# Kernel optimization log

Measured on AMD Instinct MI355X. Metric: run time of the kernel, lower is better.

Reference implementation:

```python
import jax, jax.numpy as jnp
import numpy as np

HIDDEN = 256  # C
STE = 128     # D

def setup_inputs() -> dict:
    key = jax.random.key(0)
    ks = jax.random.split(key, 11)
    B, P, Q, N = 8, 96, 96, 1024
    s = 0.02
    return {
        "enc": jax.random.normal(ks[0], (B, P, N, HIDDEN), jnp.float32),
        "ste_enc": jax.random.normal(ks[1], (B, P, N, STE), jnp.float32),
        "ste_dec": jax.random.normal(ks[2], (B, Q, N, STE), jnp.float32),
        "Wq": jax.random.normal(ks[3], (STE, HIDDEN), jnp.float32) * s,
        "bq": jnp.zeros((HIDDEN,), jnp.float32),
        "Wk": jax.random.normal(ks[4], (STE, HIDDEN), jnp.float32) * s,
        "bk": jnp.zeros((HIDDEN,), jnp.float32),
        "Wv": jax.random.normal(ks[5], (HIDDEN, HIDDEN), jnp.float32) * s,
        "bv": jnp.zeros((HIDDEN,), jnp.float32),
        "Wo": jax.random.normal(ks[6], (HIDDEN, HIDDEN), jnp.float32) * s,
        "bo": jnp.zeros((HIDDEN,), jnp.float32),
    }

def reference(enc, ste_enc, ste_dec, Wq, bq, Wk, bk, Wv, bv, Wo, bo):
    # enc: (B,P,N,C), ste_enc: (B,P,N,D), ste_dec: (B,Q,N,D)
    C = enc.shape[-1]
    q = ste_dec @ Wq + bq          # (B,Q,N,H)
    k = ste_enc @ Wk + bk          # (B,P,N,H)
    v = enc @ Wv + bv              # (B,P,N,H)
    # attention per (batch, node): scores (B,N,Q,P)
    scores = jnp.einsum("bqnh,bpnh->bnqp", q, k) / jnp.sqrt(jnp.float32(C))
    attn = jax.nn.softmax(scores, axis=-1)
    out = jnp.einsum("bnqp,bpnh->bqnh", attn, v)  # (B,Q,N,H)
    out = out @ Wo + bo
    return out  # (B,Q,N,C)
```

## Files before the change

### kernel.cpp

```cpp
#include <hip/hip_runtime.h>
#include <stdint.h>

typedef unsigned short u16;
typedef unsigned int u32;
typedef __attribute__((ext_vector_type(8))) short short8;
typedef __attribute__((ext_vector_type(4))) float f32x4;

#define NTHR 384
#define K2E16 0.09016844005556021f

#define KW_OFF    32768
#define KW_STRIDE 272
#define BIAS_OFF  58880
#define BVO_OFF   59264
#define LDS_TOTAL 60288

static __device__ __forceinline__ u16 f2bf(float f) {
  union { float f; u32 u; } v; v.f = f;
  u32 r = v.u + 0x7FFFu + ((v.u >> 16) & 1u);
  return (u16)(r >> 16);
}

__global__ __launch_bounds__(256) void k_setup(
    const float* __restrict__ Wq, const float* __restrict__ Wk,
    const float* __restrict__ Wv, const float* __restrict__ Wo,
    const float* __restrict__ bq,
    const float* __restrict__ bv, const float* __restrict__ bo,
    u16* __restrict__ WkqF, u16* __restrict__ WvoF, float* __restrict__ bvo) {
  const int ci = blockIdx.x;
  const int co = threadIdx.x;
  float acc = 0.f;
  for (int h = 0; h < 256; ++h) acc += Wv[ci*256 + h] * Wo[h*256 + co];
  const int lanepart = ((ci >> 3) & 3)*16 + (co & 15), e = ci & 7;
  const int idxv = (((ci >> 5)*16 + (co >> 4))*64 + lanepart)*8 + e;
  WvoF[idxv] = f2bf(acc);
  if (ci < 128 && co < 144) {
    float a = 0.f;
    if (co < 128)       { for (int h = 0; h < 256; ++h) a += Wk[ci*256 + h] * Wq[co*256 + h]; }
    else if (co == 128) { for (int h = 0; h < 256; ++h) a += Wk[ci*256 + h] * bq[h]; }
    const int idx = (((ci >> 5)*9 + (co >> 4))*64 + lanepart)*8 + e;
    WkqF[idx] = f2bf(a);
  }
  if (ci == 0) {
    float a2 = 0.f;
    for (int h = 0; h < 256; ++h) a2 += bv[h] * Wo[h*256 + co];
    bvo[co] = a2 + bo[co];
  }
}

__global__ __launch_bounds__(NTHR, 3) void k_attn(
    const float* __restrict__ sdec, const float* __restrict__ senc,
    const float* __restrict__ enc,
    const u16* __restrict__ WkqF, const u16* __restrict__ WvoF,
    const float* __restrict__ bvo, float* __restrict__ out) {
  extern __shared__ char smem[];
  char* wvoL   = smem;
  char* kwL    = smem + KW_OFF;
  char* fragA  = smem + KW_OFF;
  char* fragB  = smem;
  float* biasL = (float*)(smem + BIAS_OFF);
  float* bvoL  = (float*)(smem + BVO_OFF);

  const int n = blockIdx.x, b = blockIdx.y;
  const int tid = threadIdx.x, wave = tid >> 6, lane = tid & 63;
  const int g = lane >> 4, c15 = lane & 15;
  const int prow = 16*wave + c15;

  const float* sdp = sdec + ((size_t)((b*96 + prow)*1024 + n))*128 + 8*g;
  const float* sep = senc + ((size_t)((b*96 + prow)*1024 + n))*128 + 8*g;
  float4 sdv[4][2], sev[4][2];
  #pragma unroll
  for (int kt = 0; kt < 4; ++kt) {
    sev[kt][0] = *(const float4*)(sep + 32*kt);
    sev[kt][1] = *(const float4*)(sep + 32*kt + 4);
    sdv[kt][0] = *(const float4*)(sdp + 32*kt);
    sdv[kt][1] = *(const float4*)(sdp + 32*kt + 4);
  }
  const f32x4* wv = (const f32x4*)WvoF;
  f32x4 c0[3];
  #pragma unroll
  for (int i = 0; i < 3; ++i) {
    const int idx = tid + 384*i;
    if (idx < 1024) c0[i] = wv[idx];
  }
  if (tid < 256) bvoL[tid] = bvo[tid];

  short8 sef[4], sdf[4];
  #pragma unroll
  for (int kt = 0; kt < 4; ++kt) {
    union { u32 u[4]; short8 v; } cv;
    cv.u[0] = (u32)f2bf(sev[kt][0].x) | ((u32)f2bf(sev[kt][0].y) << 16);
    cv.u[1] = (u32)f2bf(sev[kt][0].z) | ((u32)f2bf(sev[kt][0].w) << 16);
    cv.u[2] = (u32)f2bf(sev[kt][1].x) | ((u32)f2bf(sev[kt][1].y) << 16);
    cv.u[3] = (u32)f2bf(sev[kt][1].z) | ((u32)f2bf(sev[kt][1].w) << 16);
    sef[kt] = cv.v;
  }
  #pragma unroll
  for (int kt = 0; kt < 4; ++kt) {
    union { u32 u[4]; short8 v; } cv;
    cv.u[0] = (u32)f2bf(sdv[kt][0].x) | ((u32)f2bf(sdv[kt][0].y) << 16);
    cv.u[1] = (u32)f2bf(sdv[kt][0].z) | ((u32)f2bf(sdv[kt][0].w) << 16);
    cv.u[2] = (u32)f2bf(sdv[kt][1].x) | ((u32)f2bf(sdv[kt][1].y) << 16);
    cv.u[3] = (u32)f2bf(sdv[kt][1].z) | ((u32)f2bf(sdv[kt][1].w) << 16);
    sdf[kt] = cv.v;
  }

  {
    f32x4 acc[9];
    #pragma unroll
    for (int nt = 0; nt < 9; ++nt) acc[nt] = (f32x4)0.f;
    #pragma unroll
    for (int kt = 0; kt < 4; ++kt) {
      #pragma unroll
      for (int nt = 0; nt < 9; ++nt) {
        const short8 bf = *(const short8*)(WkqF + (size_t)((kt*9 + nt)*64 + lane)*8);
        acc[nt] = __builtin_amdgcn_mfma_f32_16x16x32_bf16(sef[kt], bf, acc[nt], 0, 0, 0);
      }
    }
    #pragma unroll
    for (int nt = 0; nt < 8; ++nt) {
      #pragma unroll
      for (int r = 0; r < 4; ++r)
        *(u16*)(kwL + (16*wave + 4*g + r)*KW_STRIDE + 2*(c15 + 16*nt)) = f2bf(acc[nt][r]);
    }
    if (c15 == 0) {
      #pragma unroll
      for (int r = 0; r < 4; ++r) biasL[16*wave + 4*g + r] = acc[8][r];
    }
  }
  {
    f32x4* b0 = (f32x4*)wvoL;
    #pragma unroll
    for (int i = 0; i < 3; ++i) {
      const int idx = tid + 384*i;
      if (idx < 1024) b0[idx] = c0[i];
    }
  }
  __syncthreads();

  const float* ep = enc + ((size_t)((b*96 + prow)*1024 + n))*256 + 8*g;
  float4 ev[8][2];
  #pragma unroll
  for (int kt = 0; kt < 8; ++kt) {
    ev[kt][0] = *(const float4*)(ep + 32*kt);
    ev[kt][1] = *(const float4*)(ep + 32*kt + 4);
  }

  f32x4 sac[6];
  #pragma unroll
  for (int pt = 0; pt < 6; ++pt) sac[pt] = (f32x4)0.f;
  #pragma unroll
  for (int kt = 0; kt < 4; ++kt) {
    #pragma unroll
    for (int pt = 0; pt < 6; ++pt) {
      const short8 kf = *(const short8*)(kwL + (16*pt + c15)*KW_STRIDE + 16*g + 64*kt);
      sac[pt] = __builtin_amdgcn_mfma_f32_16x16x32_bf16(kf, sdf[kt], sac[pt], 0, 0, 0);
    }
  }
  #pragma unroll
  for (int pt = 0; pt < 6; ++pt)
    #pragma unroll
    for (int r = 0; r < 4; ++r)
      sac[pt][r] += biasL[16*pt + 4*g + r];

  float m = sac[0][0];
  #pragma unroll
  for (int pt = 0; pt < 6; ++pt)
    #pragma unroll
    for (int r = 0; r < 4; ++r) m = fmaxf(m, sac[pt][r]);
  m = fmaxf(m, __shfl_xor(m, 16));
  m = fmaxf(m, __shfl_xor(m, 32));
  float s = 0.f;
  #pragma unroll
  for (int pt = 0; pt < 6; ++pt)
    #pragma unroll
    for (int r = 0; r < 4; ++r) {
      const float e = exp2f((sac[pt][r] - m) * K2E16);
      sac[pt][r] = e; s += e;
    }
  s += __shfl_xor(s, 16);
  s += __shfl_xor(s, 32);
  const float rs = 1.f / s;

  short8 af[3];
  #pragma unroll
  for (int kb = 0; kb < 3; ++kb) {
    union { u32 u[4]; short8 v; } cv;
    cv.u[0] = (u32)f2bf(sac[2*kb][0]*rs)   | ((u32)f2bf(sac[2*kb][1]*rs)   << 16);
    cv.u[1] = (u32)f2bf(sac[2*kb][2]*rs)   | ((u32)f2bf(sac[2*kb][3]*rs)   << 16);
    cv.u[2] = (u32)f2bf(sac[2*kb+1][0]*rs) | ((u32)f2bf(sac[2*kb+1][1]*rs) << 16);
    cv.u[3] = (u32)f2bf(sac[2*kb+1][2]*rs) | ((u32)f2bf(sac[2*kb+1][3]*rs) << 16);
    af[kb] = cv.v;
  }

  f32x4 acc2[16];
  #pragma unroll
  for (int nt = 0; nt < 16; ++nt) acc2[nt] = (f32x4)0.f;
  #pragma unroll
  for (int kt = 0; kt < 8; ++kt) {
    f32x4 nx[3];
    if (kt < 7) {
      const f32x4* src = wv + (kt + 1)*1024;
      #pragma unroll
      for (int i = 0; i < 3; ++i) {
        const int idx = tid + 384*i;
        if (idx < 1024) nx[i] = src[idx];
      }
    }
    union { u32 u[4]; short8 v; } cv;
    cv.u[0] = (u32)f2bf(ev[kt][0].x) | ((u32)f2bf(ev[kt][0].y) << 16);
    cv.u[1] = (u32)f2bf(ev[kt][0].z) | ((u32)f2bf(ev[kt][0].w) << 16);
    cv.u[2] = (u32)f2bf(ev[kt][1].x) | ((u32)f2bf(ev[kt][1].y) << 16);
    cv.u[3] = (u32)f2bf(ev[kt][1].z) | ((u32)f2bf(ev[kt][1].w) << 16);
    const short8 a = cv.v;
    const char* buf = wvoL + (kt & 1)*16384;
    #pragma unroll
    for (int nt = 0; nt < 16; ++nt) {
      const short8 bf = *(const short8*)(buf + ((nt*64 + lane) << 4));
      acc2[nt] = __builtin_amdgcn_mfma_f32_16x16x32_bf16(a, bf, acc2[nt], 0, 0, 0);
    }
    if (kt < 7) {
      f32x4* bw = (f32x4*)(wvoL + ((kt + 1) & 1)*16384);
      #pragma unroll
      for (int i = 0; i < 3; ++i) {
        const int idx = tid + 384*i;
        if (idx < 1024) bw[idx] = nx[i];
      }
    }
    __syncthreads();
  }

  const int kb0 = wave >> 1, hi = wave & 1;
  #pragma unroll
  for (int ntl = 0; ntl < 8; ++ntl) {
    uint2 oA, oB;
    const f32x4 vA = acc2[ntl], vB = acc2[8 + ntl];
    oA.x = (u32)f2bf(vA[0]) | ((u32)f2bf(vA[1]) << 16);
    oA.y = (u32)f2bf(vA[2]) | ((u32)f2bf(vA[3]) << 16);
    oB.x = (u32)f2bf(vB[0]) | ((u32)f2bf(vB[1]) << 16);
    oB.y = (u32)f2bf(vB[2]) | ((u32)f2bf(vB[3]) << 16);
    *(uint2*)(fragA + (((ntl*3 + kb0)*64 + lane) << 4) + hi*8) = oA;
    *(uint2*)(fragB + (((ntl*3 + kb0)*64 + lane) << 4) + hi*8) = oB;
  }
  __syncthreads();

  #pragma unroll
  for (int nt = 0; nt < 16; ++nt) {
    const char* fb = (nt < 8) ? fragA : fragB;
    const int ntl = nt & 7;
    f32x4 oa = (f32x4)0.f;
    #pragma unroll
    for (int kb = 0; kb < 3; ++kb) {
      const short8 ef = *(const short8*)(fb + (((ntl*3 + kb)*64 + lane) << 4));
      oa = __builtin_amdgcn_mfma_f32_16x16x32_bf16(af[kb], ef, oa, 0, 0, 0);
    }
    const int c = c15 + 16*nt;
    const float bz = bvoL[c];
    #pragma unroll
    for (int r = 0; r < 4; ++r) {
      const int qi = 16*wave + 4*g + r;
      out[((size_t)((b*96 + qi)*1024 + n))*256 + c] = oa[r] + bz;
    }
  }
}

extern "C" void kernel_launch(void* const* d_in, const int* in_sizes, int n_in,
                              void* d_out, int out_size, void* d_ws, size_t ws_size,
                              hipStream_t stream) {
  const float* enc     = (const float*)d_in[0];
  const float* ste_enc = (const float*)d_in[1];
  const float* ste_dec = (const float*)d_in[2];
  const float* Wq = (const float*)d_in[3];
  const float* bq = (const float*)d_in[4];
  const float* Wk = (const float*)d_in[5];
  const float* Wv = (const float*)d_in[7];
  const float* bv = (const float*)d_in[8];
  const float* Wo = (const float*)d_in[9];
  const float* bo = (const float*)d_in[10];
  float* out = (float*)d_out;

  u16*   WkqF = (u16*)d_ws;
  u16*   WvoF = (u16*)((char*)d_ws + 36864);
  float* bvo  = (float*)((char*)d_ws + 167936);

  k_setup<<<dim3(256), dim3(256), 0, stream>>>(Wq, Wk, Wv, Wo, bq, bv, bo,
                                               WkqF, WvoF, bvo);
  k_attn<<<dim3(1024, 8), dim3(NTHR), LDS_TOTAL, stream>>>(
      ste_dec, ste_enc, enc, WkqF, WvoF, bvo, out);
}
```

Measured before the change: 684.5 us.

## Halve LDS footprint by streaming Wvo in half-chunks and splitting output stage

The Wvo weight staging buffer is cut from two 16KB halves to two 8KB halves by streaming the V·O weights in 16 half-k-tile chunks. The final attention-times-V stage is also split into two halves that reuse a single fragment buffer. Total LDS drops from about 60KB to about 44KB, which could allow more resident blocks per CU. The cost is twice as many barrier-separated iterations in the main GEMM loop plus an extra sync in the epilogue.

```diff
diff --git a/kernel.cpp b/kernel.cpp
--- a/kernel.cpp
+++ b/kernel.cpp
@@ -9,11 +9,11 @@
 #define NTHR 384
 #define K2E16 0.09016844005556021f
 
-#define KW_OFF    32768
+#define KW_OFF    16384
 #define KW_STRIDE 272
-#define BIAS_OFF  58880
-#define BVO_OFF   59264
-#define LDS_TOTAL 60288
+#define BIAS_OFF  42496
+#define BVO_OFF   42880
+#define LDS_TOTAL 43904
 
 static __device__ __forceinline__ u16 f2bf(float f) {
   union { float f; u32 u; } v; v.f = f;
@@ -56,8 +56,7 @@
   extern __shared__ char smem[];
   char* wvoL   = smem;
   char* kwL    = smem + KW_OFF;
-  char* fragA  = smem + KW_OFF;
-  char* fragB  = smem;
+  char* fragH  = smem + KW_OFF;
   float* biasL = (float*)(smem + BIAS_OFF);
   float* bvoL  = (float*)(smem + BVO_OFF);
 
@@ -77,12 +76,9 @@
     sdv[kt][1] = *(const float4*)(sdp + 32*kt + 4);
   }
   const f32x4* wv = (const f32x4*)WvoF;
-  f32x4 c0[3];
-  #pragma unroll
-  for (int i = 0; i < 3; ++i) {
-    const int idx = tid + 384*i;
-    if (idx < 1024) c0[i] = wv[idx];
-  }
+  f32x4 c0a, c0b;
+  c0a = wv[tid];
+  if (tid < 128) c0b = wv[384 + tid];
   if (tid < 256) bvoL[tid] = bvo[tid];
 
   short8 sef[4], sdf[4];
@@ -130,11 +126,8 @@
   }
   {
     f32x4* b0 = (f32x4*)wvoL;
-    #pragma unroll
-    for (int i = 0; i < 3; ++i) {
-      const int idx = tid + 384*i;
-      if (idx < 1024) b0[idx] = c0[i];
-    }
+    b0[tid] = c0a;
+    if (tid < 128) b0[384 + tid] = c0b;
   }
   __syncthreads();
 
@@ -196,71 +189,68 @@
   f32x4 acc2[16];
   #pragma unroll
   for (int nt = 0; nt < 16; ++nt) acc2[nt] = (f32x4)0.f;
-  #pragma unroll
-  for (int kt = 0; kt < 8; ++kt) {
-    f32x4 nx[3];
-    if (kt < 7) {
-      const f32x4* src = wv + (kt + 1)*1024;
-      #pragma unroll
-      for (int i = 0; i < 3; ++i) {
-        const int idx = tid + 384*i;
-        if (idx < 1024) nx[i] = src[idx];
+  short8 acur;
+  #pragma unroll
+  for (int ci = 0; ci < 16; ++ci) {
+    f32x4 nxa, nxb;
+    if (ci < 15) {
+      const f32x4* src = wv + (ci + 1)*512;
+      nxa = src[tid];
+      if (tid < 128) nxb = src[384 + tid];
+    }
+    if ((ci & 1) == 0) {
+      const int kt = ci >> 1;
+      union { u32 u[4]; short8 v; } cv;
+      cv.u[0] = (u32)f2bf(ev[kt][0].x) | ((u32)f2bf(ev[kt][0].y) << 16);
+      cv.u[1] = (u32)f2bf(ev[kt][0].z) | ((u32)f2bf(ev[kt][0].w) << 16);
+      cv.u[2] = (u32)f2bf(ev[kt][1].x) | ((u32)f2bf(ev[kt][1].y) << 16);
+      cv.u[3] = (u32)f2bf(ev[kt][1].z) | ((u32)f2bf(ev[kt][1].w) << 16);
+      acur = cv.v;
+    }
+    const char* buf = wvoL + (ci & 1)*8192;
+    const int ntb = (ci & 1)*8;
+    #pragma unroll
+    for (int ntl = 0; ntl < 8; ++ntl) {
+      const short8 bf = *(const short8*)(buf + ((ntl*64 + lane) << 4));
+      acc2[ntb + ntl] = __builtin_amdgcn_mfma_f32_16x16x32_bf16(acur, bf, acc2[ntb + ntl], 0, 0, 0);
+    }
+    if (ci < 15) {
+      f32x4* bw = (f32x4*)(wvoL + ((ci + 1) & 1)*8192);
+      bw[tid] = nxa;
+      if (tid < 128) bw[384 + tid] = nxb;
+    }
+    __syncthreads();
+  }
+
+  const int kb0 = wave >> 1, hi = wave & 1;
+  #pragma unroll
+  for (int half = 0; half < 2; ++half) {
+    #pragma unroll
+    for (int ntl = 0; ntl < 8; ++ntl) {
+      uint2 o;
+      const f32x4 v = acc2[half*8 + ntl];
+      o.x = (u32)f2bf(v[0]) | ((u32)f2bf(v[1]) << 16);
+      o.y = (u32)f2bf(v[2]) | ((u32)f2bf(v[3]) << 16);
+      *(uint2*)(fragH + (((ntl*3 + kb0)*64 + lane) << 4) + hi*8) = o;
+    }
+    __syncthreads();
+    #pragma unroll
+    for (int ntl = 0; ntl < 8; ++ntl) {
+      f32x4 oa = (f32x4)0.f;
+      #pragma unroll
+      for (int kb = 0; kb < 3; ++kb) {
+        const short8 ef = *(const short8*)(fragH + (((ntl*3 + kb)*64 + lane) << 4));
+        oa = __builtin_amdgcn_mfma_f32_16x16x32_bf16(af[kb], ef, oa, 0, 0, 0);
       }
-    }
-    union { u32 u[4]; short8 v; } cv;
-    cv.u[0] = (u32)f2bf(ev[kt][0].x) | ((u32)f2bf(ev[kt][0].y) << 16);
-    cv.u[1] = (u32)f2bf(ev[kt][0].z) | ((u32)f2bf(ev[kt][0].w) << 16);
-    cv.u[2] = (u32)f2bf(ev[kt][1].x) | ((u32)f2bf(ev[kt][1].y) << 16);
-    cv.u[3] = (u32)f2bf(ev[kt][1].z) | ((u32)f2bf(ev[kt][1].w) << 16);
-    const short8 a = cv.v;
-    const char* buf = wvoL + (kt & 1)*16384;
-    #pragma unroll
-    for (int nt = 0; nt < 16; ++nt) {
-      const short8 bf = *(const short8*)(buf + ((nt*64 + lane) << 4));
-      acc2[nt] = __builtin_amdgcn_mfma_f32_16x16x32_bf16(a, bf, acc2[nt], 0, 0, 0);
-    }
-    if (kt < 7) {
-      f32x4* bw = (f32x4*)(wvoL + ((kt + 1) & 1)*16384);
-      #pragma unroll
-      for (int i = 0; i < 3; ++i) {
-        const int idx = tid + 384*i;
-        if (idx < 1024) bw[idx] = nx[i];
+      const int c = c15 + 16*(half*8 + ntl);
+      const float bz = bvoL[c];
+      #pragma unroll
+      for (int r = 0; r < 4; ++r) {
+        const int qi = 16*wave + 4*g + r;
+        out[((size_t)((b*96 + qi)*1024 + n))*256 + c] = oa[r] + bz;
       }
     }
-    __syncthreads();
-  }
-
-  const int kb0 = wave >> 1, hi = wave & 1;
-  #pragma unroll
-  for (int ntl = 0; ntl < 8; ++ntl) {
-    uint2 oA, oB;
-    const f32x4 vA = acc2[ntl], vB = acc2[8 + ntl];
-    oA.x = (u32)f2bf(vA[0]) | ((u32)f2bf(vA[1]) << 16);
-    oA.y = (u32)f2bf(vA[2]) | ((u32)f2bf(vA[3]) << 16);
-    oB.x = (u32)f2bf(vB[0]) | ((u32)f2bf(vB[1]) << 16);
-    oB.y = (u32)f2bf(vB[2]) | ((u32)f2bf(vB[3]) << 16);
-    *(uint2*)(fragA + (((ntl*3 + kb0)*64 + lane) << 4) + hi*8) = oA;
-    *(uint2*)(fragB + (((ntl*3 + kb0)*64 + lane) << 4) + hi*8) = oB;
-  }
-  __syncthreads();
-
-  #pragma unroll
-  for (int nt = 0; nt < 16; ++nt) {
-    const char* fb = (nt < 8) ? fragA : fragB;
-    const int ntl = nt & 7;
-    f32x4 oa = (f32x4)0.f;
-    #pragma unroll
-    for (int kb = 0; kb < 3; ++kb) {
-      const short8 ef = *(const short8*)(fb + (((ntl*3 + kb)*64 + lane) << 4));
-      oa = __builtin_amdgcn_mfma_f32_16x16x32_bf16(af[kb], ef, oa, 0, 0, 0);
-    }
-    const int c = c15 + 16*nt;
-    const float bz = bvoL[c];
-    #pragma unroll
-    for (int r = 0; r < 4; ++r) {
-      const int qi = 16*wave + 4*g + r;
-      out[((size_t)((b*96 + qi)*1024 + n))*256 + c] = oa[r] + bz;
-    }
+    if (half == 0) __syncthreads();
   }
 }
 
```

Measured after the change: 803.8 us. +17.4%, slower.
